# Optimization experiments

Hardware: AMD Instinct MI355X
Metric: run time of the kernel (lower is better)

The kernel has to match this reference:

```python
import jax, jax.numpy as jnp
import numpy as np

B, N, NV, P, S, H, DE, DO, NCLS = 128, 64, 14, 32, 14, 128, 64, 64, 5


def _edge_indices(n):
    # all ordered pairs (r, s), r != s — same order as itertools.product with diagonal removed
    idx = np.array([(r, s) for r in range(n) for s in range(n) if r != s], dtype=np.int32)
    return jnp.asarray(idx[:, 0]), jnp.asarray(idx[:, 1])


def _lin(key, fin, fout):
    kw, kb = jax.random.split(key)
    lim = 1.0 / np.sqrt(fin)
    w = jax.random.uniform(kw, (fin, fout), jnp.float32, -lim, lim)
    b = jax.random.uniform(kb, (fout,), jnp.float32, -lim, lim)
    return w, b


def _mlp3(h, w1, b1, w2, b2, w3, b3):
    h = jax.nn.relu(h @ w1 + b1)
    h = jax.nn.relu(h @ w2 + b2)
    return jax.nn.relu(h @ w3 + b3)


def setup_inputs() -> dict:
    key = jax.random.key(0)
    ks = jax.random.split(key, 12)
    inp = {
        'x': jax.random.normal(ks[0], (B, P, N), jnp.float32),
        'y': jax.random.normal(ks[1], (B, S, NV), jnp.float32),
    }
    inp['fr1_w'], inp['fr1_b'] = _lin(ks[2], 2 * P, H)
    inp['fr2_w'], inp['fr2_b'] = _lin(ks[3], H, H)
    inp['fr3_w'], inp['fr3_b'] = _lin(ks[4], H, DE)
    inp['fr1pv_w'], inp['fr1pv_b'] = _lin(ks[5], P + S, H)
    inp['fr2pv_w'], inp['fr2pv_b'] = _lin(ks[6], H, H)
    inp['fr3pv_w'], inp['fr3pv_b'] = _lin(ks[7], H, DE)
    inp['fo1_w'], inp['fo1_b'] = _lin(ks[8], P + 2 * DE, H)
    inp['fo2_w'], inp['fo2_b'] = _lin(ks[9], H, H)
    inp['fo3_w'], inp['fo3_b'] = _lin(ks[10], H, DO)
    inp['fc_w'], inp['fc_b'] = _lin(ks[11], DO, NCLS)
    return inp


def reference(x, y, fr1_w, fr1_b, fr2_w, fr2_b, fr3_w, fr3_b,
              fr1pv_w, fr1pv_b, fr2pv_w, fr2pv_b, fr3pv_w, fr3pv_b,
              fo1_w, fo1_b, fo2_w, fo2_b, fo3_w, fo3_b, fc_w, fc_b):
    b, p, n = x.shape
    nv = y.shape[2]
    de = fr3_w.shape[1]
    xT = jnp.transpose(x, (0, 2, 1))  # [B, N, P]
    yT = jnp.transpose(y, (0, 2, 1))  # [B, Nv, S]

    # particle-particle edges: one-hot Rr/Rs matmuls == gather by (receiver, sender)
    r_idx, s_idx = _edge_indices(n)
    epp_in = jnp.concatenate([xT[:, r_idx], xT[:, s_idx]], axis=-1)  # [B, Nr, 2P]
    E_pp = _mlp3(epp_in, fr1_w, fr1_b, fr2_w, fr2_b, fr3_w, fr3_b)   # [B, Nr, De]
    # E @ Rr^T == scatter-add onto receivers
    Ebar_pp = jnp.zeros((b, n, de), x.dtype).at[:, r_idx].add(E_pp)  # [B, N, De]

    # particle-vertex edges: Rk/Rv one-hot gathers over product(N, Nv)
    k_idx = jnp.repeat(jnp.arange(n), nv)
    v_idx = jnp.tile(jnp.arange(nv), n)
    epv_in = jnp.concatenate([xT[:, k_idx], yT[:, v_idx]], axis=-1)  # [B, Nt, P+S]
    E_pv = _mlp3(epv_in, fr1pv_w, fr1pv_b, fr2pv_w, fr2pv_b, fr3pv_w, fr3pv_b)
    Ebar_pv = jnp.zeros((b, n, de), x.dtype).at[:, k_idx].add(E_pv)  # [B, N, De]
    # (the torch code also computes Ebar_vp = E @ Rv^T but never uses it)

    C = jnp.concatenate([xT, Ebar_pp, Ebar_pv], axis=-1)  # [B, N, P+2De]
    O = _mlp3(C, fo1_w, fo1_b, fo2_w, fo2_b, fo3_w, fo3_b)  # [B, N, Do]
    pooled = jnp.sum(O, axis=1)  # [B, Do]
    return pooled @ fc_w + fc_b  # [B, n_targets]
```

## Files before the change

### kernel.cpp

```cpp
#include <hip/hip_runtime.h>

typedef __attribute__((ext_vector_type(8))) _Float16 half8;
typedef __attribute__((ext_vector_type(4))) _Float16 half4v;
typedef __attribute__((ext_vector_type(4))) float floatx4;

#define NB 128
#define NN 64
#define NV 14
#define PP 32
#define SS 14
#define HH 128
#define DE 64
#define NCLS 5
#define PITCH 136

#define OFF_W2   0
#define OFF_W3   16384
#define OFF_W2PV 24576
#define OFF_W3PV 40960
#define OFF_FO1  49152
#define OFF_FO2  69632
#define OFF_FO3  86016

__device__ __forceinline__ floatx4 MFMA(half8 a, half8 b, floatx4 c) {
  return __builtin_amdgcn_mfma_f32_16x16x32_f16(a, b, c, 0, 0, 0);
}

__global__ __launch_bounds__(256) void k0_prep(
    const float* __restrict__ x, const float* __restrict__ y,
    const float* __restrict__ fr1_w, const float* __restrict__ fr1_b,
    const float* __restrict__ fr1pv_w, const float* __restrict__ fr1pv_b,
    const float* __restrict__ fr2_w, const float* __restrict__ fr3_w,
    const float* __restrict__ fr2pv_w, const float* __restrict__ fr3pv_w,
    const float* __restrict__ fo1_w, const float* __restrict__ fo2_w,
    const float* __restrict__ fo3_w,
    _Float16* __restrict__ A1h, _Float16* __restrict__ B1h,
    _Float16* __restrict__ A1pvh, _Float16* __restrict__ B1pvh,
    _Float16* __restrict__ WT, float* __restrict__ dout) {
  int blk = blockIdx.x;
  int tid = threadIdx.x;
  if (blk < 768) {
    int mat = blk >> 8, sub = blk & 255;
    int b = sub >> 1, n0 = (sub & 1) << 5;
    __shared__ float sxT[32 * 33];
    for (int i = tid; i < 32 * PP; i += 256) {
      int p = i >> 5, n = i & 31;
      sxT[n * 33 + p] = x[b * (PP * NN) + p * 64 + n0 + n];
    }
    __syncthreads();
    const float* w; _Float16* outp; const float* bias;
    if (mat == 0)      { w = fr1_w;           outp = A1h;   bias = fr1_b; }
    else if (mat == 1) { w = fr1_w + 32 * HH; outp = B1h;   bias = nullptr; }
    else               { w = fr1pv_w;         outp = A1pvh; bias = fr1pv_b; }
    for (int o = tid; o < 32 * 32; o += 256) {
      int n = o >> 5, jc = o & 31;
      float4 acc = {0.f, 0.f, 0.f, 0.f};
      const float* xr = &sxT[n * 33];
#pragma unroll 8
      for (int k = 0; k < PP; k++) {
        float xv = xr[k];
        float4 wv = ((const float4*)w)[k * 32 + jc];
        acc.x += xv * wv.x; acc.y += xv * wv.y;
        acc.z += xv * wv.z; acc.w += xv * wv.w;
      }
      if (bias) {
        float4 bv = ((const float4*)bias)[jc];
        acc.x += bv.x; acc.y += bv.y; acc.z += bv.z; acc.w += bv.w;
      }
      half4v hv;
      hv[0] = (_Float16)acc.x; hv[1] = (_Float16)acc.y;
      hv[2] = (_Float16)acc.z; hv[3] = (_Float16)acc.w;
      *(half4v*)(&outp[(b * NN + n0 + n) * HH + jc * 4]) = hv;
    }
  } else if (blk < 896) {
    int b = blk - 768;
    __shared__ float syT[NV * 15];
    for (int i = tid; i < SS * NV; i += 256) {
      int s = i / NV, v = i - s * NV;
      syT[v * 15 + s] = y[b * (SS * NV) + i];
    }
    __syncthreads();
    const float4* w4 = (const float4*)(fr1pv_w + 32 * HH);
    for (int o = tid; o < NV * 32; o += 256) {
      int v = o >> 5, jc = o & 31;
      float4 acc = {0.f, 0.f, 0.f, 0.f};
#pragma unroll
      for (int s = 0; s < SS; s++) {
        float yv = syT[v * 15 + s];
        float4 wv = w4[s * 32 + jc];
        acc.x += yv * wv.x; acc.y += yv * wv.y;
        acc.z += yv * wv.z; acc.w += yv * wv.w;
      }
      half4v hv;
      hv[0] = (_Float16)acc.x; hv[1] = (_Float16)acc.y;
      hv[2] = (_Float16)acc.z; hv[3] = (_Float16)acc.w;
      *(half4v*)(&B1pvh[(b * NV + v) * HH + jc * 4]) = hv;
    }
  } else if (blk < 925) {
    int t = blk - 896;
    int wid, ks;
    if (t < 16)      { wid = t >> 2; ks = t & 3; }
    else if (t < 21) { wid = 4; ks = t - 16; }
    else if (t < 25) { wid = 5; ks = t - 21; }
    else             { wid = 6; ks = t - 25; }
    const float* src; int N, NKS, NTN; _Float16* dst;
    switch (wid) {
      case 0: src = fr2_w;   N = 128; NKS = 4; NTN = 8; dst = WT + OFF_W2;   break;
      case 1: src = fr3_w;   N = 64;  NKS = 4; NTN = 4; dst = WT + OFF_W3;   break;
      case 2: src = fr2pv_w; N = 128; NKS = 4; NTN = 8; dst = WT + OFF_W2PV; break;
      case 3: src = fr3pv_w; N = 64;  NKS = 4; NTN = 4; dst = WT + OFF_W3PV; break;
      case 4: src = fo1_w;   N = 128; NKS = 5; NTN = 8; dst = WT + OFF_FO1;  break;
      case 5: src = fo2_w;   N = 128; NKS = 4; NTN = 8; dst = WT + OFF_FO2;  break;
      default: src = fo3_w;  N = 64;  NKS = 4; NTN = 4; dst = WT + OFF_FO3;  break;
    }
    __shared__ float sw[32 * 132];
    int NP = N + 4;
    int n4 = N >> 2;
    for (int i = tid; i < 32 * n4; i += 256) {
      int row = i / n4, c4 = i - row * n4;
      *(float4*)(&sw[row * NP + c4 * 4]) = *(const float4*)(&src[(ks * 32 + row) * N + c4 * 4]);
    }
    __syncthreads();
    for (int o = tid; o < NTN * 64; o += 256) {
      int nt = o >> 6, l = o & 63;
      int cc = l & 15, qq = l >> 4;
      half8 hv;
#pragma unroll
      for (int j = 0; j < 8; j++) hv[j] = (_Float16)sw[(qq * 8 + j) * NP + nt * 16 + cc];
      *(half8*)(&dst[((nt * NKS + ks) * 64 + l) << 3]) = hv;
    }
  } else {
    for (int i = tid; i < NB * NCLS; i += 256) dout[i] = 0.f;
  }
}

template <int NPAIRS, int NR, int DIV, int RRMAX, bool SKIP>
__device__ __forceinline__ void edge_body(
    const _Float16* __restrict__ Ab,
    const _Float16* __restrict__ Bb,
    const _Float16* sW2,
    const _Float16* __restrict__ w3g,
    const float* sB2, const float* sB3,
    _Float16* sH, float* sEb, int r0, int lane, int wv) {
  int c = lane & 15, q = lane >> 4;
#pragma unroll 1
  for (int tp = 0; tp < NPAIRS; tp++) {
    int z0 = 0;
    asm volatile("" : "+v"(z0));
    int tb0 = ((wv * NPAIRS + tp) << 5);
    int tb1 = tb0 + 16;
    int rowl0 = tb0 + c;
    int rr0 = rowl0 / DIV; if (rr0 > RRMAX) rr0 = RRMAX;
    int jj0 = rowl0 - rr0 * DIV; if (jj0 > DIV - 1) jj0 = DIV - 1;
    int s0 = SKIP ? (jj0 + (jj0 >= r0 + rr0 ? 1 : 0)) : jj0;
    int rowl1 = tb1 + c;
    int rr1 = rowl1 / DIV; if (rr1 > RRMAX) rr1 = RRMAX;
    int jj1 = rowl1 - rr1 * DIV; if (jj1 > DIV - 1) jj1 = DIV - 1;
    int s1 = SKIP ? (jj1 + (jj1 >= r0 + rr1 ? 1 : 0)) : jj1;
    const _Float16* a0p = Ab + rr0 * HH;
    const _Float16* b0p = Bb + s0 * HH;
    const _Float16* a1p = Ab + rr1 * HH;
    const _Float16* b1p = Bb + s1 * HH;
    floatx4 acc0[8], acc1[8];
#pragma unroll
    for (int nt = 0; nt < 8; nt++) {
      acc0[nt] = (floatx4){0.f, 0.f, 0.f, 0.f};
      acc1[nt] = (floatx4){0.f, 0.f, 0.f, 0.f};
    }
#pragma unroll
    for (int ks = 0; ks < 4; ks++) {
      half8 av0 = *(const half8*)(a0p + ks * 32 + q * 8);
      half8 bv0 = *(const half8*)(b0p + ks * 32 + q * 8);
      half8 av1 = *(const half8*)(a1p + ks * 32 + q * 8);
      half8 bv1 = *(const half8*)(b1p + ks * 32 + q * 8);
      half8 h0 = av0 + bv0;
      half8 h1 = av1 + bv1;
#pragma unroll
      for (int j = 0; j < 8; j++) {
        h0[j] = h0[j] > (_Float16)0.f ? h0[j] : (_Float16)0.f;
        h1[j] = h1[j] > (_Float16)0.f ? h1[j] : (_Float16)0.f;
      }
#pragma unroll
      for (int nt = 0; nt < 8; nt++) {
        half8 w = *(const half8*)(&sW2[z0 + ((nt * 4 + ks) << 9) + (lane << 3)]);
        acc0[nt] = MFMA(w, h0, acc0[nt]);
        acc1[nt] = MFMA(w, h1, acc1[nt]);
      }
    }
    half4v g1r[8];
#pragma unroll
    for (int nt = 0; nt < 8; nt++) {
      float4 bbt = *(const float4*)(&sB2[z0 + nt * 16 + q * 4]);
      half4v g0, g1;
      g0[0] = (_Float16)fmaxf(acc0[nt][0] + bbt.x, 0.f);
      g0[1] = (_Float16)fmaxf(acc0[nt][1] + bbt.y, 0.f);
      g0[2] = (_Float16)fmaxf(acc0[nt][2] + bbt.z, 0.f);
      g0[3] = (_Float16)fmaxf(acc0[nt][3] + bbt.w, 0.f);
      g1[0] = (_Float16)fmaxf(acc1[nt][0] + bbt.x, 0.f);
      g1[1] = (_Float16)fmaxf(acc1[nt][1] + bbt.y, 0.f);
      g1[2] = (_Float16)fmaxf(acc1[nt][2] + bbt.z, 0.f);
      g1[3] = (_Float16)fmaxf(acc1[nt][3] + bbt.w, 0.f);
      int slot = ((nt << 1) + (q >> 1)) ^ c;
      int addr = (c << 7) + (slot << 3) + ((q & 1) << 2);
      *(half4v*)(&sH[addr]) = g0;
      g1r[nt] = g1;
    }
    half8 a20[4], a21[4];
#pragma unroll
    for (int ks = 0; ks < 4; ks++) {
      int addr = (c << 7) + ((((ks << 2) + q) ^ c) << 3);
      a20[ks] = *(const half8*)(&sH[addr]);
    }
#pragma unroll
    for (int nt = 0; nt < 8; nt++) {
      int slot = ((nt << 1) + (q >> 1)) ^ c;
      int addr = (c << 7) + (slot << 3) + ((q & 1) << 2);
      *(half4v*)(&sH[addr]) = g1r[nt];
    }
#pragma unroll
    for (int ks = 0; ks < 4; ks++) {
      int addr = (c << 7) + ((((ks << 2) + q) ^ c) << 3);
      a21[ks] = *(const half8*)(&sH[addr]);
    }
#pragma unroll
    for (int nt3 = 0; nt3 < 4; nt3++) {
      floatx4 e0 = {0.f, 0.f, 0.f, 0.f};
      floatx4 e1 = {0.f, 0.f, 0.f, 0.f};
#pragma unroll
      for (int ks = 0; ks < 4; ks++) {
        half8 wf = *(const half8*)(&w3g[z0 + ((nt3 * 4 + ks) << 9) + (lane << 3)]);
        e0 = MFMA(a20[ks], wf, e0);
        e1 = MFMA(a21[ks], wf, e1);
      }
      float bb3v = sB3[z0 + nt3 * 16 + c];
      int col = nt3 * 16 + c;
#pragma unroll
      for (int half_ = 0; half_ < 2; half_++) {
        floatx4 e = half_ ? e1 : e0;
        int rbase = (half_ ? tb1 : tb0) + q * 4;
        if (rbase < NR) {
          float v0 = fmaxf(e[0] + bb3v, 0.f);
          float v1 = fmaxf(e[1] + bb3v, 0.f);
          float v2 = fmaxf(e[2] + bb3v, 0.f);
          float v3 = fmaxf(e[3] + bb3v, 0.f);
          int rrA = rbase / DIV, rrB = (rbase + 3) / DIV;
          if (rrA == rrB && rbase + 3 < NR) {
            atomicAdd(&sEb[rrA * 64 + col], v0 + v1 + v2 + v3);
          } else {
            float vs[4] = {v0, v1, v2, v3};
#pragma unroll
            for (int rg = 0; rg < 4; rg++) {
              int r2 = rbase + rg;
              if (r2 < NR) atomicAdd(&sEb[(r2 / DIV) * 64 + col], vs[rg]);
            }
          }
        }
      }
    }
  }
}

#define PPB2 (NB * 4)
#define EGRID2 (NB * 4 + NB * 2)
__global__ __launch_bounds__(256, 2) void edge_fused(
    const _Float16* __restrict__ A1h, const _Float16* __restrict__ B1h,
    const _Float16* __restrict__ A1pvh, const _Float16* __restrict__ B1pvh,
    const float* __restrict__ fr2_b, const float* __restrict__ fr3_b,
    const float* __restrict__ fr2pv_b, const float* __restrict__ fr3pv_b,
    const _Float16* __restrict__ WT,
    float* __restrict__ Epp, float* __restrict__ Epv) {
  __shared__ __align__(16) _Float16 sW2[16384];
  __shared__ __align__(16) _Float16 sH2s[4][2048];
  __shared__ __align__(16) float sEb[512];
  __shared__ __align__(16) float sB2[128];
  __shared__ __align__(16) float sB3[64];
  int tid = threadIdx.x;
  int lane = tid & 63, wv = tid >> 6;
  bool ispp = blockIdx.x < PPB2;
  const _Float16* w2src = ispp ? (WT + OFF_W2) : (WT + OFF_W2PV);
  for (int i = tid; i < 2048; i += 256)
    *(uint4*)(&sW2[i * 8]) = *(const uint4*)(&w2src[i * 8]);
  const float* b2g = ispp ? fr2_b : fr2pv_b;
  const float* b3g = ispp ? fr3_b : fr3pv_b;
  if (tid < 128) sB2[tid] = b2g[tid];
  else if (tid < 192) sB3[tid - 128] = b3g[tid - 128];
  if (ispp) {
    int b = blockIdx.x >> 2, c4 = blockIdx.x & 3;
#pragma unroll 1
    for (int g = 0; g < 4; g++) {
      int r0 = c4 * 16 + g * 4;
      for (int i = tid; i < 512; i += 256) sEb[i] = 0.f;
      __syncthreads();
      edge_body<2, 252, 63, 3, true>(
          A1h + (b * NN + r0) * HH, B1h + b * NN * HH,
          sW2, WT + OFF_W3, sB2, sB3,
          &sH2s[wv][0], sEb, r0, lane, wv);
      __syncthreads();
      Epp[(b * NN + r0 + (tid >> 6)) * DE + (tid & 63)] = sEb[tid];
    }
  } else {
    int p = blockIdx.x - PPB2;
    int b = p >> 1, hf2 = p & 1;
#pragma unroll 1
    for (int g = 0; g < 4; g++) {
      int k0g = (hf2 * 4 + g) * 8;
      for (int i = tid; i < 512; i += 256) sEb[i] = 0.f;
      __syncthreads();
      edge_body<1, 112, 14, 7, false>(
          A1pvh + (b * NN + k0g) * HH, B1pvh + b * NV * HH,
          sW2, WT + OFF_W3PV, sB2, sB3,
          &sH2s[wv][0], sEb, 0, lane, wv);
      __syncthreads();
      for (int i = tid; i < 512; i += 256)
        Epv[(b * NN + k0g + (i >> 6)) * DE + (i & 63)] = sEb[i];
    }
  }
}

__global__ __launch_bounds__(256) void node_out(
    const float* __restrict__ x, const float* __restrict__ Epp,
    const float* __restrict__ Epv,
    const float* __restrict__ fo1_b, const float* __restrict__ fo2_b,
    const float* __restrict__ fo3_b,
    const float* __restrict__ fc_w, const float* __restrict__ fc_b,
    const _Float16* __restrict__ WT, float* __restrict__ out) {
  __shared__ _Float16 sC[16 * 168];
  __shared__ _Float16 sHa[16 * PITCH];
  __shared__ _Float16 sHb[16 * PITCH];
  __shared__ float sPool[64];
  int tid = threadIdx.x;
  int b = blockIdx.x >> 2, r0 = (blockIdx.x & 3) << 4;
  for (int i = tid; i < 16 * 32; i += 256) {
    int row = i >> 5, p = i & 31;
    sC[row * 168 + p] = (_Float16)x[b * (PP * NN) + p * 64 + r0 + row];
  }
  for (int i = tid; i < 16 * 16; i += 256) {
    int row = i >> 4, d4 = i & 15;
    float4 vpp = *(const float4*)(&Epp[(b * NN + r0 + row) * DE + d4 * 4]);
    float4 vpv = *(const float4*)(&Epv[(b * NN + r0 + row) * DE + d4 * 4]);
    half4v hpp, hpv;
    hpp[0] = (_Float16)vpp.x; hpp[1] = (_Float16)vpp.y;
    hpp[2] = (_Float16)vpp.z; hpp[3] = (_Float16)vpp.w;
    hpv[0] = (_Float16)vpv.x; hpv[1] = (_Float16)vpv.y;
    hpv[2] = (_Float16)vpv.z; hpv[3] = (_Float16)vpv.w;
    *(half4v*)(&sC[row * 168 + 32 + d4 * 4]) = hpp;
    *(half4v*)(&sC[row * 168 + 96 + d4 * 4]) = hpv;
  }
  __syncthreads();
  int lane = tid & 63, wv = tid >> 6;
  int c = lane & 15, q = lane >> 4;
  half8 cf[5];
#pragma unroll
  for (int ks = 0; ks < 5; ks++)
    cf[ks] = *(const half8*)(&sC[c * 168 + ks * 32 + q * 8]);
#pragma unroll
  for (int nt2 = 0; nt2 < 2; nt2++) {
    int nt = wv * 2 + nt2;
    floatx4 a0 = {0.f, 0.f, 0.f, 0.f};
#pragma unroll
    for (int ks = 0; ks < 5; ks++) {
      half8 wf = *(const half8*)(&WT[OFF_FO1 + ((nt * 5 + ks) << 9) + (lane << 3)]);
      a0 = MFMA(wf, cf[ks], a0);
    }
    float4 bb = *(const float4*)(&fo1_b[nt * 16 + q * 4]);
    half4v h0;
    h0[0] = (_Float16)fmaxf(a0[0] + bb.x, 0.f);
    h0[1] = (_Float16)fmaxf(a0[1] + bb.y, 0.f);
    h0[2] = (_Float16)fmaxf(a0[2] + bb.z, 0.f);
    h0[3] = (_Float16)fmaxf(a0[3] + bb.w, 0.f);
    *(half4v*)(&sHa[c * PITCH + nt * 16 + q * 4]) = h0;
  }
  __syncthreads();
  half8 g1[4];
#pragma unroll
  for (int ks = 0; ks < 4; ks++)
    g1[ks] = *(const half8*)(&sHa[c * PITCH + ks * 32 + q * 8]);
#pragma unroll
  for (int nt2 = 0; nt2 < 2; nt2++) {
    int nt = wv * 2 + nt2;
    floatx4 a0 = {0.f, 0.f, 0.f, 0.f};
#pragma unroll
    for (int ks = 0; ks < 4; ks++) {
      half8 wf = *(const half8*)(&WT[OFF_FO2 + ((nt * 4 + ks) << 9) + (lane << 3)]);
      a0 = MFMA(wf, g1[ks], a0);
    }
    float4 bb = *(const float4*)(&fo2_b[nt * 16 + q * 4]);
    half4v h0;
    h0[0] = (_Float16)fmaxf(a0[0] + bb.x, 0.f);
    h0[1] = (_Float16)fmaxf(a0[1] + bb.y, 0.f);
    h0[2] = (_Float16)fmaxf(a0[2] + bb.z, 0.f);
    h0[3] = (_Float16)fmaxf(a0[3] + bb.w, 0.f);
    *(half4v*)(&sHb[c * PITCH + nt * 16 + q * 4]) = h0;
  }
  __syncthreads();
  half8 g2[4];
#pragma unroll
  for (int ks = 0; ks < 4; ks++)
    g2[ks] = *(const half8*)(&sHb[c * PITCH + ks * 32 + q * 8]);
  floatx4 e0 = {0.f, 0.f, 0.f, 0.f};
#pragma unroll
  for (int ks = 0; ks < 4; ks++) {
    half8 wf = *(const half8*)(&WT[OFF_FO3 + ((wv * 4 + ks) << 9) + (lane << 3)]);
    e0 = MFMA(g2[ks], wf, e0);
  }
  float bb3 = fo3_b[wv * 16 + c];
  float s = 0.f;
#pragma unroll
  for (int rg = 0; rg < 4; rg++) s += fmaxf(e0[rg] + bb3, 0.f);
  s += __shfl_xor(s, 16);
  s += __shfl_xor(s, 32);
  if (lane < 16) sPool[wv * 16 + c] = s;
  __syncthreads();
  if (tid < NCLS) {
    float o = ((blockIdx.x & 3) == 0) ? fc_b[tid] : 0.f;
#pragma unroll
    for (int d = 0; d < 64; d++) o += sPool[d] * fc_w[d * NCLS + tid];
    atomicAdd(&out[b * NCLS + tid], o);
  }
}

extern "C" void kernel_launch(void* const* d_in, const int* in_sizes, int n_in,
                              void* d_out, int out_size, void* d_ws, size_t ws_size,
                              hipStream_t stream) {
  const float* x = (const float*)d_in[0];
  const float* y = (const float*)d_in[1];
  const float* fr1_w = (const float*)d_in[2];  const float* fr1_b = (const float*)d_in[3];
  const float* fr2_w = (const float*)d_in[4];  const float* fr2_b = (const float*)d_in[5];
  const float* fr3_w = (const float*)d_in[6];  const float* fr3_b = (const float*)d_in[7];
  const float* fr1pv_w = (const float*)d_in[8];  const float* fr1pv_b = (const float*)d_in[9];
  const float* fr2pv_w = (const float*)d_in[10]; const float* fr2pv_b = (const float*)d_in[11];
  const float* fr3pv_w = (const float*)d_in[12]; const float* fr3pv_b = (const float*)d_in[13];
  const float* fo1_w = (const float*)d_in[14];  const float* fo1_b = (const float*)d_in[15];
  const float* fo2_w = (const float*)d_in[16];  const float* fo2_b = (const float*)d_in[17];
  const float* fo3_w = (const float*)d_in[18];  const float* fo3_b = (const float*)d_in[19];
  const float* fc_w = (const float*)d_in[20];   const float* fc_b = (const float*)d_in[21];

  char* ws = (char*)d_ws;
  _Float16* A1h   = (_Float16*)(ws);
  _Float16* B1h   = (_Float16*)(ws + (2u << 20));
  _Float16* A1pvh = (_Float16*)(ws + (4u << 20));
  _Float16* B1pvh = (_Float16*)(ws + (6u << 20));
  _Float16* WT    = (_Float16*)(ws + (7u << 20));
  float* Epp      = (float*)(ws + (8u << 20));
  float* Epv      = (float*)(ws + (10u << 20));

  k0_prep<<<926, 256, 0, stream>>>(x, y, fr1_w, fr1_b, fr1pv_w, fr1pv_b,
                                   fr2_w, fr3_w, fr2pv_w, fr3pv_w,
                                   fo1_w, fo2_w, fo3_w,
                                   A1h, B1h, A1pvh, B1pvh, WT, (float*)d_out);
  edge_fused<<<EGRID2, 256, 0, stream>>>(A1h, B1h, A1pvh, B1pvh,
                                         fr2_b, fr3_b, fr2pv_b, fr3pv_b,
                                         WT, Epp, Epv);
  node_out<<<NB * 4, 256, 0, stream>>>(x, Epp, Epv, fo1_b, fo2_b, fo3_b,
                                       fc_w, fc_b, WT, (float*)d_out);
}
```

Before: 204.8 us.

## Assign one receiver per wave and reduce edges in registers instead of LDS atomics

Each wave now owns whole receivers: pp waves process all 63 senders of one receiver and pv waves all 14 vertices of one particle. The aggregation is done with register accumulation plus cross-lane shuffles, and the result is written directly to global memory. This removes the shared-memory atomicAdd scatter, the sEb buffer and the per-group block barriers, and loads the receiver row once per wave. The pv path now uses a single 16-row tile per particle, which leaves 2 of its 16 rows idle and wastes MFMA work on that padding.

After: 165.2 us (median of 2 runs). 1.24x faster.

```diff
diff --git a/kernel.cpp b/kernel.cpp
--- a/kernel.cpp
+++ b/kernel.cpp
@@ -134,32 +134,27 @@
   }
 }
 
-template <int NPAIRS, int NR, int DIV, int RRMAX, bool SKIP>
-__device__ __forceinline__ void edge_body(
-    const _Float16* __restrict__ Ab,
-    const _Float16* __restrict__ Bb,
-    const _Float16* sW2,
-    const _Float16* __restrict__ w3g,
+__device__ __forceinline__ void pp_wave(
+    const _Float16* __restrict__ Arow, const _Float16* __restrict__ Bb,
+    const _Float16* sW2, const _Float16* __restrict__ w3g,
     const float* sB2, const float* sB3,
-    _Float16* sH, float* sEb, int r0, int lane, int wv) {
+    _Float16* sH, int r, int lane, float* __restrict__ outp) {
   int c = lane & 15, q = lane >> 4;
+  half8 av[4];
+#pragma unroll
+  for (int ks = 0; ks < 4; ks++)
+    av[ks] = *(const half8*)(Arow + ks * 32 + q * 8);
+  floatx4 regS = {0.f, 0.f, 0.f, 0.f};
 #pragma unroll 1
-  for (int tp = 0; tp < NPAIRS; tp++) {
+  for (int tp = 0; tp < 2; tp++) {
     int z0 = 0;
     asm volatile("" : "+v"(z0));
-    int tb0 = ((wv * NPAIRS + tp) << 5);
-    int tb1 = tb0 + 16;
-    int rowl0 = tb0 + c;
-    int rr0 = rowl0 / DIV; if (rr0 > RRMAX) rr0 = RRMAX;
-    int jj0 = rowl0 - rr0 * DIV; if (jj0 > DIV - 1) jj0 = DIV - 1;
-    int s0 = SKIP ? (jj0 + (jj0 >= r0 + rr0 ? 1 : 0)) : jj0;
-    int rowl1 = tb1 + c;
-    int rr1 = rowl1 / DIV; if (rr1 > RRMAX) rr1 = RRMAX;
-    int jj1 = rowl1 - rr1 * DIV; if (jj1 > DIV - 1) jj1 = DIV - 1;
-    int s1 = SKIP ? (jj1 + (jj1 >= r0 + rr1 ? 1 : 0)) : jj1;
-    const _Float16* a0p = Ab + rr0 * HH;
+    int tb0 = tp * 32, tb1 = tb0 + 16;
+    int jj0 = tb0 + c; if (jj0 > 62) jj0 = 62;
+    int s0 = jj0 + (jj0 >= r ? 1 : 0);
+    int jj1 = tb1 + c; if (jj1 > 62) jj1 = 62;
+    int s1 = jj1 + (jj1 >= r ? 1 : 0);
     const _Float16* b0p = Bb + s0 * HH;
-    const _Float16* a1p = Ab + rr1 * HH;
     const _Float16* b1p = Bb + s1 * HH;
     floatx4 acc0[8], acc1[8];
 #pragma unroll
@@ -169,12 +164,10 @@
     }
 #pragma unroll
     for (int ks = 0; ks < 4; ks++) {
-      half8 av0 = *(const half8*)(a0p + ks * 32 + q * 8);
       half8 bv0 = *(const half8*)(b0p + ks * 32 + q * 8);
-      half8 av1 = *(const half8*)(a1p + ks * 32 + q * 8);
       half8 bv1 = *(const half8*)(b1p + ks * 32 + q * 8);
-      half8 h0 = av0 + bv0;
-      half8 h1 = av1 + bv1;
+      half8 h0 = av[ks] + bv0;
+      half8 h1 = av[ks] + bv1;
 #pragma unroll
       for (int j = 0; j < 8; j++) {
         h0[j] = h0[j] > (_Float16)0.f ? h0[j] : (_Float16)0.f;
@@ -232,36 +225,98 @@
         e0 = MFMA(a20[ks], wf, e0);
         e1 = MFMA(a21[ks], wf, e1);
       }
-      float bb3v = sB3[z0 + nt3 * 16 + c];
-      int col = nt3 * 16 + c;
-#pragma unroll
-      for (int half_ = 0; half_ < 2; half_++) {
-        floatx4 e = half_ ? e1 : e0;
-        int rbase = (half_ ? tb1 : tb0) + q * 4;
-        if (rbase < NR) {
-          float v0 = fmaxf(e[0] + bb3v, 0.f);
-          float v1 = fmaxf(e[1] + bb3v, 0.f);
-          float v2 = fmaxf(e[2] + bb3v, 0.f);
-          float v3 = fmaxf(e[3] + bb3v, 0.f);
-          int rrA = rbase / DIV, rrB = (rbase + 3) / DIV;
-          if (rrA == rrB && rbase + 3 < NR) {
-            atomicAdd(&sEb[rrA * 64 + col], v0 + v1 + v2 + v3);
-          } else {
-            float vs[4] = {v0, v1, v2, v3};
-#pragma unroll
-            for (int rg = 0; rg < 4; rg++) {
-              int r2 = rbase + rg;
-              if (r2 < NR) atomicAdd(&sEb[(r2 / DIV) * 64 + col], vs[rg]);
-            }
-          }
-        }
-      }
-    }
-  }
-}
-
-#define PPB2 (NB * 4)
-#define EGRID2 (NB * 4 + NB * 2)
+      float b3v = sB3[z0 + nt3 * 16 + c];
+      int rb0 = tb0 + q * 4, rb1 = tb1 + q * 4;
+#pragma unroll
+      for (int rg = 0; rg < 4; rg++) {
+        if (rb0 + rg < 63) regS[nt3] += fmaxf(e0[rg] + b3v, 0.f);
+        if (rb1 + rg < 63) regS[nt3] += fmaxf(e1[rg] + b3v, 0.f);
+      }
+    }
+  }
+  float t0 = regS[0], t1 = regS[1], t2 = regS[2], t3 = regS[3];
+  t0 += __shfl_xor(t0, 16); t0 += __shfl_xor(t0, 32);
+  t1 += __shfl_xor(t1, 16); t1 += __shfl_xor(t1, 32);
+  t2 += __shfl_xor(t2, 16); t2 += __shfl_xor(t2, 32);
+  t3 += __shfl_xor(t3, 16); t3 += __shfl_xor(t3, 32);
+  float v = q == 0 ? t0 : (q == 1 ? t1 : (q == 2 ? t2 : t3));
+  outp[q * 16 + c] = v;
+}
+
+__device__ __forceinline__ void pv_wave(
+    const _Float16* __restrict__ Arow, const _Float16* __restrict__ Bb,
+    const _Float16* sW2, const _Float16* __restrict__ w3g,
+    const float* sB2, const float* sB3,
+    _Float16* sH, int lane, float* __restrict__ outp) {
+  int c = lane & 15, q = lane >> 4;
+  int z0 = 0;
+  asm volatile("" : "+v"(z0));
+  int v14 = c > 13 ? 13 : c;
+  const _Float16* bp = Bb + v14 * HH;
+  half8 av[4];
+#pragma unroll
+  for (int ks = 0; ks < 4; ks++)
+    av[ks] = *(const half8*)(Arow + ks * 32 + q * 8);
+  floatx4 acc[8];
+#pragma unroll
+  for (int nt = 0; nt < 8; nt++) acc[nt] = (floatx4){0.f, 0.f, 0.f, 0.f};
+#pragma unroll
+  for (int ks = 0; ks < 4; ks++) {
+    half8 bv = *(const half8*)(bp + ks * 32 + q * 8);
+    half8 h = av[ks] + bv;
+#pragma unroll
+    for (int j = 0; j < 8; j++) h[j] = h[j] > (_Float16)0.f ? h[j] : (_Float16)0.f;
+#pragma unroll
+    for (int nt = 0; nt < 8; nt++) {
+      half8 w = *(const half8*)(&sW2[z0 + ((nt * 4 + ks) << 9) + (lane << 3)]);
+      acc[nt] = MFMA(w, h, acc[nt]);
+    }
+  }
+#pragma unroll
+  for (int nt = 0; nt < 8; nt++) {
+    float4 bbt = *(const float4*)(&sB2[z0 + nt * 16 + q * 4]);
+    half4v g0;
+    g0[0] = (_Float16)fmaxf(acc[nt][0] + bbt.x, 0.f);
+    g0[1] = (_Float16)fmaxf(acc[nt][1] + bbt.y, 0.f);
+    g0[2] = (_Float16)fmaxf(acc[nt][2] + bbt.z, 0.f);
+    g0[3] = (_Float16)fmaxf(acc[nt][3] + bbt.w, 0.f);
+    int slot = ((nt << 1) + (q >> 1)) ^ c;
+    int addr = (c << 7) + (slot << 3) + ((q & 1) << 2);
+    *(half4v*)(&sH[addr]) = g0;
+  }
+  half8 a2[4];
+#pragma unroll
+  for (int ks = 0; ks < 4; ks++) {
+    int addr = (c << 7) + ((((ks << 2) + q) ^ c) << 3);
+    a2[ks] = *(const half8*)(&sH[addr]);
+  }
+  floatx4 regS = {0.f, 0.f, 0.f, 0.f};
+#pragma unroll
+  for (int nt3 = 0; nt3 < 4; nt3++) {
+    floatx4 e = {0.f, 0.f, 0.f, 0.f};
+#pragma unroll
+    for (int ks = 0; ks < 4; ks++) {
+      half8 wf = *(const half8*)(&w3g[z0 + ((nt3 * 4 + ks) << 9) + (lane << 3)]);
+      e = MFMA(a2[ks], wf, e);
+    }
+    float b3v = sB3[z0 + nt3 * 16 + c];
+    int rb = q * 4;
+#pragma unroll
+    for (int rg = 0; rg < 4; rg++) {
+      if (rb + rg < 14) regS[nt3] += fmaxf(e[rg] + b3v, 0.f);
+    }
+  }
+  float t0 = regS[0], t1 = regS[1], t2 = regS[2], t3 = regS[3];
+  t0 += __shfl_xor(t0, 16); t0 += __shfl_xor(t0, 32);
+  t1 += __shfl_xor(t1, 16); t1 += __shfl_xor(t1, 32);
+  t2 += __shfl_xor(t2, 16); t2 += __shfl_xor(t2, 32);
+  t3 += __shfl_xor(t3, 16); t3 += __shfl_xor(t3, 32);
+  float v = q == 0 ? t0 : (q == 1 ? t1 : (q == 2 ? t2 : t3));
+  outp[q * 16 + c] = v;
+}
+
+#define PPB3 (NB * 4)
+#define EGRID3 (NB * 4 + NB * 2)
 __global__ __launch_bounds__(256, 2) void edge_fused(
     const _Float16* __restrict__ A1h, const _Float16* __restrict__ B1h,
     const _Float16* __restrict__ A1pvh, const _Float16* __restrict__ B1pvh,
@@ -271,12 +326,11 @@
     float* __restrict__ Epp, float* __restrict__ Epv) {
   __shared__ __align__(16) _Float16 sW2[16384];
   __shared__ __align__(16) _Float16 sH2s[4][2048];
-  __shared__ __align__(16) float sEb[512];
   __shared__ __align__(16) float sB2[128];
   __shared__ __align__(16) float sB3[64];
   int tid = threadIdx.x;
   int lane = tid & 63, wv = tid >> 6;
-  bool ispp = blockIdx.x < PPB2;
+  bool ispp = blockIdx.x < PPB3;
   const _Float16* w2src = ispp ? (WT + OFF_W2) : (WT + OFF_W2PV);
   for (int i = tid; i < 2048; i += 256)
     *(uint4*)(&sW2[i * 8]) = *(const uint4*)(&w2src[i * 8]);
@@ -284,35 +338,25 @@
   const float* b3g = ispp ? fr3_b : fr3pv_b;
   if (tid < 128) sB2[tid] = b2g[tid];
   else if (tid < 192) sB3[tid - 128] = b3g[tid - 128];
+  __syncthreads();
   if (ispp) {
-    int b = blockIdx.x >> 2, c4 = blockIdx.x & 3;
+    int b = blockIdx.x >> 2, r0 = (blockIdx.x & 3) << 4;
 #pragma unroll 1
-    for (int g = 0; g < 4; g++) {
-      int r0 = c4 * 16 + g * 4;
-      for (int i = tid; i < 512; i += 256) sEb[i] = 0.f;
-      __syncthreads();
-      edge_body<2, 252, 63, 3, true>(
-          A1h + (b * NN + r0) * HH, B1h + b * NN * HH,
-          sW2, WT + OFF_W3, sB2, sB3,
-          &sH2s[wv][0], sEb, r0, lane, wv);
-      __syncthreads();
-      Epp[(b * NN + r0 + (tid >> 6)) * DE + (tid & 63)] = sEb[tid];
+    for (int rcv = 0; rcv < 4; rcv++) {
+      int r = r0 + wv * 4 + rcv;
+      pp_wave(A1h + (b * NN + r) * HH, B1h + b * NN * HH,
+              sW2, WT + OFF_W3, sB2, sB3,
+              &sH2s[wv][0], r, lane, Epp + (b * NN + r) * DE);
     }
   } else {
-    int p = blockIdx.x - PPB2;
+    int p = blockIdx.x - PPB3;
     int b = p >> 1, hf2 = p & 1;
 #pragma unroll 1
-    for (int g = 0; g < 4; g++) {
-      int k0g = (hf2 * 4 + g) * 8;
-      for (int i = tid; i < 512; i += 256) sEb[i] = 0.f;
-      __syncthreads();
-      edge_body<1, 112, 14, 7, false>(
-          A1pvh + (b * NN + k0g) * HH, B1pvh + b * NV * HH,
-          sW2, WT + OFF_W3PV, sB2, sB3,
-          &sH2s[wv][0], sEb, 0, lane, wv);
-      __syncthreads();
-      for (int i = tid; i < 512; i += 256)
-        Epv[(b * NN + k0g + (i >> 6)) * DE + (i & 63)] = sEb[i];
+    for (int kk = 0; kk < 8; kk++) {
+      int k = hf2 * 32 + wv * 8 + kk;
+      pv_wave(A1pvh + (b * NN + k) * HH, B1pvh + b * NV * HH,
+              sW2, WT + OFF_W3PV, sB2, sB3,
+              &sH2s[wv][0], lane, Epv + (b * NN + k) * DE);
     }
   }
 }
@@ -448,7 +492,7 @@
                                    fr2_w, fr3_w, fr2pv_w, fr3pv_w,
                                    fo1_w, fo2_w, fo3_w,
                                    A1h, B1h, A1pvh, B1pvh, WT, (float*)d_out);
-  edge_fused<<<EGRID2, 256, 0, stream>>>(A1h, B1h, A1pvh, B1pvh,
+  edge_fused<<<EGRID3, 256, 0, stream>>>(A1h, B1h, A1pvh, B1pvh,
                                          fr2_b, fr3_b, fr2pv_b, fr3pv_b,
                                          WT, Epp, Epv);
   node_out<<<NB * 4, 256, 0, stream>>>(x, Epp, Epv, fo1_b, fo2_b, fo3_b,
```
